# Optimization experiments

Measured on AMD Instinct MI355X. Metric: run time of the kernel, lower is better.

## Reference

```python
import jax, jax.numpy as jnp
import numpy as np

RADIX = 16
INPUT_SIZE = 4096  # 16**3 -> 3 recursion levels
# residual flags per level, replicating the source quirk:
# level0: residual=True -> bool(True)=True, passes int(True)-1 = 0
# level1: residual=0    -> bool(0)=False,   passes int(0)-1   = -1
# level2: residual=-1   -> bool(-1)=True (negative ints are truthy)
RES_FLAGS = (True, False, True)


def _butterfly(x, weights, lins, res_flags):
    """Faithful vectorized translation of OptimisedRNNFFT.forward.

    x: (..., N); weights: list of per-level vectors (N, N/r, ...);
    lins: list of (radix, radix) matrices; res_flags: per-level residual bools.
    """
    n = x.shape[-1]
    chunk = n // RADIX
    if n > RADIX:
        # recurse on radix-sized chunks of the last dim
        xr = x.reshape(*x.shape[:-1], RADIX, chunk)
        y = _butterfly(xr, weights[1:], lins[1:], res_flags[1:])
        y = y.reshape(*x.shape[:-1], n)
    else:
        y = x  # Identity at the base level
    y = weights[0] * y                                   # elementwise weighting
    yb = y.reshape(*y.shape[:-1], RADIX, chunk)          # (..., radix, chunk)
    r = jnp.einsum('ij,...jc->...ic', lins[0], yb)       # radix x radix mix
    r = r.reshape(*y.shape[:-1], n)
    if res_flags[0]:
        r = r + x
    return r


def setup_inputs() -> dict:
    key = jax.random.key(0)
    k = jax.random.split(key, 8)
    x = jax.random.normal(k[0], (8192, INPUT_SIZE), dtype=jnp.float32)
    # per-level elementwise weights (torch init: ones/sqrt(N); randomized here)
    w0 = jax.random.normal(k[1], (4096,), dtype=jnp.float32) / np.sqrt(4096.0)
    w1 = jax.random.normal(k[2], (256,), dtype=jnp.float32) / np.sqrt(256.0)
    w2 = jax.random.normal(k[3], (16,), dtype=jnp.float32) / np.sqrt(16.0)
    # per-level radix x radix butterfly matrices (xavier-normal-ish)
    xav = np.sqrt(2.0 / (RADIX + RADIX))
    l0 = jax.random.normal(k[4], (RADIX, RADIX), dtype=jnp.float32) * xav
    l1 = jax.random.normal(k[5], (RADIX, RADIX), dtype=jnp.float32) * xav
    l2 = jax.random.normal(k[6], (RADIX, RADIX), dtype=jnp.float32) * xav
    return {"x": x, "w0": w0, "w1": w1, "w2": w2, "l0": l0, "l1": l1, "l2": l2}


def reference(x, w0, w1, w2, l0, l1, l2):
    return _butterfly(x, [w0, w1, w2], [l0, l1, l2], RES_FLAGS)
```

## Files before the change

kernel.cpp:

```cpp
#include <hip/hip_runtime.h>

#define N 4096

__device__ __forceinline__ int swz(int e) { return e ^ ((e >> 4) & 15); }

__global__ __launch_bounds__(256, 6) void butterfly5_kernel(
    const float* __restrict__ x,
    const float* __restrict__ w0, const float* __restrict__ w1, const float* __restrict__ w2,
    const float* __restrict__ l0, const float* __restrict__ l1, const float* __restrict__ l2,
    float* __restrict__ out)
{
    __shared__ float2 lds[N];
    const int t = threadIdx.x;
    const int b1 = t >> 4, c1 = t & 15;
    const size_t row0 = (size_t)blockIdx.x * 2;
    const float* __restrict__ xA = x + row0 * N;
    const float* __restrict__ xB = xA + N;
    float* __restrict__ oA = out + row0 * N;
    float* __restrict__ oB = oA + N;

    float vA[16], vB[16];
    {
        const float4* qA = (const float4*)(xA + t * 16);
        const float4* qB = (const float4*)(xB + t * 16);
        #pragma unroll
        for (int q = 0; q < 4; ++q) {
            float4 f = qA[q];
            vA[q*4+0]=f.x; vA[q*4+1]=f.y; vA[q*4+2]=f.z; vA[q*4+3]=f.w;
        }
        #pragma unroll
        for (int q = 0; q < 4; ++q) {
            float4 f = qB[q];
            vB[q*4+0]=f.x; vB[q*4+1]=f.y; vB[q*4+2]=f.z; vB[q*4+3]=f.w;
        }
    }

    float xwA[16], xwB[16];
    #pragma unroll
    for (int j = 0; j < 16; ++j) {
        float s = w2[j];
        xwA[j] = s * vA[j];
        xwB[j] = s * vB[j];
    }
    #pragma unroll
    for (int i = 0; i < 16; ++i) {
        float a = vA[i], b = vB[i];
        #pragma unroll
        for (int j = 0; j < 16; ++j) {
            float s = l2[i*16 + j];
            a = fmaf(s, xwA[j], a);
            b = fmaf(s, xwB[j], b);
        }
        lds[swz(t*16 + i)] = make_float2(a, b);
    }

    float w1c[16];
    #pragma unroll
    for (int j = 0; j < 16; ++j) w1c[j] = w1[j*16 + c1];

    float2 y1[16];
    #pragma unroll
    for (int j = 0; j < 16; ++j) {
        float2 p = lds[swz(b1*256 + j*16 + c1)];
        y1[j].x = w1c[j] * p.x;
        y1[j].y = w1c[j] * p.y;
    }
    float2 r1[16];
    #pragma unroll
    for (int i = 0; i < 16; ++i) {
        float a = 0.f, b = 0.f;
        #pragma unroll
        for (int j = 0; j < 16; ++j) {
            float s = l1[i*16 + j];
            a = fmaf(s, y1[j].x, a);
            b = fmaf(s, y1[j].y, b);
        }
        r1[i] = make_float2(a, b);
    }
    #pragma unroll
    for (int i = 0; i < 16; ++i)
        lds[swz(b1*256 + i*16 + c1)] = r1[i];

    float w0c[16], xrA[16], xrB[16];
    #pragma unroll
    for (int j = 0; j < 16; ++j) w0c[j] = w0[j*256 + t];
    #pragma unroll
    for (int i = 0; i < 16; ++i) { xrA[i] = xA[i*256 + t]; xrB[i] = xB[i*256 + t]; }

    __syncthreads();

    float2 y0[16];
    #pragma unroll
    for (int j = 0; j < 16; ++j) {
        float2 p = lds[swz(j*256 + t)];
        y0[j].x = w0c[j] * p.x;
        y0[j].y = w0c[j] * p.y;
    }
    #pragma unroll
    for (int i = 0; i < 16; ++i) {
        float a = xrA[i], b = xrB[i];
        #pragma unroll
        for (int j = 0; j < 16; ++j) {
            float s = l0[i*16 + j];
            a = fmaf(s, y0[j].x, a);
            b = fmaf(s, y0[j].y, b);
        }
        __builtin_nontemporal_store(a, &oA[i*256 + t]);
        __builtin_nontemporal_store(b, &oB[i*256 + t]);
    }
}

extern "C" void kernel_launch(void* const* d_in, const int* in_sizes, int n_in,
                              void* d_out, int out_size, void* d_ws, size_t ws_size,
                              hipStream_t stream) {
    const float* x  = (const float*)d_in[0];
    const float* w0 = (const float*)d_in[1];
    const float* w1 = (const float*)d_in[2];
    const float* w2 = (const float*)d_in[3];
    const float* l0 = (const float*)d_in[4];
    const float* l1 = (const float*)d_in[5];
    const float* l2 = (const float*)d_in[6];
    float* out = (float*)d_out;
    const int rows = in_sizes[0] / N;
    butterfly5_kernel<<<rows / 2, 256, 0, stream>>>(x, w0, w1, w2, l0, l1, l2, out);
}
```

Baseline: 68.93 us.

## Process four rows per block, prefetching second row pair during first

```diff
diff --git a/kernel.cpp b/kernel.cpp
--- a/kernel.cpp
+++ b/kernel.cpp
@@ -4,60 +4,40 @@
 
 __device__ __forceinline__ int swz(int e) { return e ^ ((e >> 4) & 15); }
 
-__global__ __launch_bounds__(256, 6) void butterfly5_kernel(
-    const float* __restrict__ x,
+template<bool BAR_BEFORE_WRITE, bool TOUCH>
+__device__ __forceinline__ void do_pair(
+    float2* lds, int t, int b1, int c1,
+    float (&vA)[16], float (&vB)[16],
+    const float* __restrict__ xA, const float* __restrict__ xB,
+    float* __restrict__ oA, float* __restrict__ oB,
     const float* __restrict__ w0, const float* __restrict__ w1, const float* __restrict__ w2,
     const float* __restrict__ l0, const float* __restrict__ l1, const float* __restrict__ l2,
-    float* __restrict__ out)
+    const float (&tC)[16], const float (&tD)[16])
 {
-    __shared__ float2 lds[N];
-    const int t = threadIdx.x;
-    const int b1 = t >> 4, c1 = t & 15;
-    const size_t row0 = (size_t)blockIdx.x * 2;
-    const float* __restrict__ xA = x + row0 * N;
-    const float* __restrict__ xB = xA + N;
-    float* __restrict__ oA = out + row0 * N;
-    float* __restrict__ oB = oA + N;
-
-    float vA[16], vB[16];
-    {
-        const float4* qA = (const float4*)(xA + t * 16);
-        const float4* qB = (const float4*)(xB + t * 16);
-        #pragma unroll
-        for (int q = 0; q < 4; ++q) {
-            float4 f = qA[q];
-            vA[q*4+0]=f.x; vA[q*4+1]=f.y; vA[q*4+2]=f.z; vA[q*4+3]=f.w;
-        }
-        #pragma unroll
-        for (int q = 0; q < 4; ++q) {
-            float4 f = qB[q];
-            vB[q*4+0]=f.x; vB[q*4+1]=f.y; vB[q*4+2]=f.z; vB[q*4+3]=f.w;
-        }
-    }
-
-    float xwA[16], xwB[16];
+    float2 r2[16];
     #pragma unroll
-    for (int j = 0; j < 16; ++j) {
-        float s = w2[j];
-        xwA[j] = s * vA[j];
-        xwB[j] = s * vB[j];
-    }
+    for (int i = 0; i < 16; ++i) r2[i] = make_float2(vA[i], vB[i]);
+    #pragma unroll
+    for (int j = 0; j < 16; ++j) { float s = w2[j]; vA[j] *= s; vB[j] *= s; }
     #pragma unroll
     for (int i = 0; i < 16; ++i) {
-        float a = vA[i], b = vB[i];
+        float a = r2[i].x, b = r2[i].y;
         #pragma unroll
         for (int j = 0; j < 16; ++j) {
             float s = l2[i*16 + j];
-            a = fmaf(s, xwA[j], a);
-            b = fmaf(s, xwB[j], b);
+            a = fmaf(s, vA[j], a);
+            b = fmaf(s, vB[j], b);
         }
-        lds[swz(t*16 + i)] = make_float2(a, b);
+        r2[i] = make_float2(a, b);
     }
+
+    if (BAR_BEFORE_WRITE) __syncthreads();
+    #pragma unroll
+    for (int i = 0; i < 16; ++i) lds[swz(t*16 + i)] = r2[i];
 
     float w1c[16];
     #pragma unroll
     for (int j = 0; j < 16; ++j) w1c[j] = w1[j*16 + c1];
-
     float2 y1[16];
     #pragma unroll
     for (int j = 0; j < 16; ++j) {
@@ -78,17 +58,18 @@
         r1[i] = make_float2(a, b);
     }
     #pragma unroll
-    for (int i = 0; i < 16; ++i)
-        lds[swz(b1*256 + i*16 + c1)] = r1[i];
+    for (int i = 0; i < 16; ++i) lds[swz(b1*256 + i*16 + c1)] = r1[i];
 
-    float w0c[16], xrA[16], xrB[16];
+    if constexpr (TOUCH) {
+        #pragma unroll
+        for (int k = 0; k < 16; ++k)
+            asm volatile("" :: "v"(tC[k]), "v"(tD[k]));
+    }
+    __syncthreads();
+
+    float w0c[16];
     #pragma unroll
     for (int j = 0; j < 16; ++j) w0c[j] = w0[j*256 + t];
-    #pragma unroll
-    for (int i = 0; i < 16; ++i) { xrA[i] = xA[i*256 + t]; xrB[i] = xB[i*256 + t]; }
-
-    __syncthreads();
-
     float2 y0[16];
     #pragma unroll
     for (int j = 0; j < 16; ++j) {
@@ -98,7 +79,7 @@
     }
     #pragma unroll
     for (int i = 0; i < 16; ++i) {
-        float a = xrA[i], b = xrB[i];
+        float a = xA[i*256 + t], b = xB[i*256 + t];
         #pragma unroll
         for (int j = 0; j < 16; ++j) {
             float s = l0[i*16 + j];
@@ -108,6 +89,59 @@
         __builtin_nontemporal_store(a, &oA[i*256 + t]);
         __builtin_nontemporal_store(b, &oB[i*256 + t]);
     }
+}
+
+__global__ __launch_bounds__(256, 4) void butterfly10_kernel(
+    const float* __restrict__ x,
+    const float* __restrict__ w0, const float* __restrict__ w1, const float* __restrict__ w2,
+    const float* __restrict__ l0, const float* __restrict__ l1, const float* __restrict__ l2,
+    float* __restrict__ out)
+{
+    __shared__ float2 lds[N];
+    const int t = threadIdx.x;
+    const int b1 = t >> 4, c1 = t & 15;
+    const size_t row0 = (size_t)blockIdx.x * 4;
+    const float* __restrict__ xA = x + row0 * N;
+    const float* __restrict__ xB = xA + N;
+    const float* __restrict__ xC = xB + N;
+    const float* __restrict__ xD = xC + N;
+    float* __restrict__ oA = out + row0 * N;
+    float* __restrict__ oB = oA + N;
+    float* __restrict__ oC = oB + N;
+    float* __restrict__ oD = oC + N;
+
+    float vA[16], vB[16], vC[16], vD[16];
+    {
+        const float4* qA = (const float4*)(xA + t * 16);
+        const float4* qB = (const float4*)(xB + t * 16);
+        const float4* qC = (const float4*)(xC + t * 16);
+        const float4* qD = (const float4*)(xD + t * 16);
+        #pragma unroll
+        for (int q = 0; q < 4; ++q) {
+            float4 f = qA[q];
+            vA[q*4+0]=f.x; vA[q*4+1]=f.y; vA[q*4+2]=f.z; vA[q*4+3]=f.w;
+        }
+        #pragma unroll
+        for (int q = 0; q < 4; ++q) {
+            float4 f = qB[q];
+            vB[q*4+0]=f.x; vB[q*4+1]=f.y; vB[q*4+2]=f.z; vB[q*4+3]=f.w;
+        }
+        #pragma unroll
+        for (int q = 0; q < 4; ++q) {
+            float4 f = qC[q];
+            vC[q*4+0]=f.x; vC[q*4+1]=f.y; vC[q*4+2]=f.z; vC[q*4+3]=f.w;
+        }
+        #pragma unroll
+        for (int q = 0; q < 4; ++q) {
+            float4 f = qD[q];
+            vD[q*4+0]=f.x; vD[q*4+1]=f.y; vD[q*4+2]=f.z; vD[q*4+3]=f.w;
+        }
+    }
+
+    do_pair<false, true >(lds, t, b1, c1, vA, vB, xA, xB, oA, oB,
+                          w0, w1, w2, l0, l1, l2, vC, vD);
+    do_pair<true,  false>(lds, t, b1, c1, vC, vD, xC, xD, oC, oD,
+                          w0, w1, w2, l0, l1, l2, vC, vD);
 }
 
 extern "C" void kernel_launch(void* const* d_in, const int* in_sizes, int n_in,
@@ -122,5 +156,5 @@
     const float* l2 = (const float*)d_in[6];
     float* out = (float*)d_out;
     const int rows = in_sizes[0] / N;
-    butterfly5_kernel<<<rows / 2, 256, 0, stream>>>(x, w0, w1, w2, l0, l1, l2, out);
+    butterfly10_kernel<<<rows / 4, 256, 0, stream>>>(x, w0, w1, w2, l0, l1, l2, out);
 }
```

Result: slower. 129.8 us (+88.3%).
